# Kernel tuning notes

Hardware: AMD Instinct MI355X
Metric: run time of the kernel (lower is better)

Reference implementation:

```python
import jax, jax.numpy as jnp
import numpy as np

B, N, D = 16, 512, 256
PH, UH, UPH = 8, 4, 4          # P_GAT heads, U_GAT heads, UP_GAT heads
P_LAYERS, U_LAYERS = 2, 1
FH, NC = 128, 2                # final hidden, num classes
N_TRAIT = 4


def setup_inputs() -> dict:
    key = jax.random.key(0)
    keys = iter(jax.random.split(key, 64))

    def rn(shape, s=0.05):
        return jax.random.normal(next(keys), shape, dtype=jnp.float32) * s

    inp = {
        "p_mask": jnp.ones((B, N), jnp.float32),
        "feature": rn((B, N, D), 1.0),
        "c_node": rn((B, 1, D), 1.0),
        "pgat_W": rn((D, D)),
        "pgat_attn": rn((PH, 2 * (D // PH))),
    }
    for i in range(1, 5):
        inp[f"up{i}_qw"] = rn((D, D))
        inp[f"up{i}_qb"] = rn((D,))
        inp[f"up{i}_kw"] = rn((D, D))
        inp[f"up{i}_kb"] = rn((D,))
        inp[f"up{i}_ow"] = rn((D, D * UPH))
        inp[f"up{i}_ob"] = rn((D,))
    inp["ugat_W"] = rn((D, D))
    inp["ugat_attn"] = rn((UH, 2 * (D // UH)))
    inp["mlp_w1"] = rn((FH, D))
    inp["mlp_b1"] = rn((FH,))
    inp["mlp_w2"] = rn((FH, FH))
    inp["mlp_b2"] = rn((FH,))
    for i in range(1, 5):
        inp[f"fcf{i}_w"] = rn((NC, FH))
        inp[f"fcf{i}_b"] = rn((NC,))
    return inp


def _mh_gat(feature, W, attn_w, n_head, num_layers, adj=None):
    """Shared math of P_GAT / U_GAT.
    attn(cat([q_i, k_j]))[..., h, h] decomposes into q_i.wq_h + k_j.wk_h,
    identical math to the broadcast-concat-linear-diagonal in the source."""
    Bx, Nx, d = feature.shape
    dh = d // n_head
    wq, wk = attn_w[:, :dh], attn_w[:, dh:]           # [h, dh] each
    for _ in range(num_layers):
        qk = (feature @ W.T).reshape(Bx, Nx, n_head, dh)
        sq = jnp.einsum('bqhd,hd->bqh', qk, wq)
        sk = jnp.einsum('bkhd,hd->bkh', qk, wk)
        scores = jnp.tanh(sq[:, :, None, :] + sk[:, None, :, :])  # [B,q,k,h]
        if adj is not None:
            scores = jnp.where(adj[:, :, :, None] == 0, jnp.float32(-1e-8), scores)
        att = jax.nn.softmax(scores, axis=-2)          # softmax over k
        hid = jnp.tanh(jnp.einsum('bqkh,bkhd->bqhd', att, qk))
        feature = feature + hid.reshape(Bx, Nx, d)
    return feature


def _up_gat(p_mask, p_feat, u_feat, qw, qb, kw, kb, ow, ob):
    """UP_GAT: all heads/layers share params & inputs -> identical heads."""
    d = p_feat.shape[-1]
    q = u_feat @ qw.T + qb                             # [B,1,D]
    k = p_feat @ kw.T + kb                             # [B,Np,D]
    sim = jnp.einsum('bqd,bkd->bqk', q, k) / jnp.sqrt(jnp.float32(d))
    sim = jnp.where(p_mask[:, None, :] == 0, jnp.float32(1e-8), sim)
    att = jax.nn.softmax(sim, axis=2)
    head = att @ p_feat                                # [B,1,D]
    mh = jnp.concatenate([head] * UPH, axis=-1)        # concat of identical heads
    return (mh @ ow.T + ob)[:, 0, :]                   # squeeze(1)


def reference(p_mask, feature, c_node, pgat_W, pgat_attn,
              up1_qw, up1_qb, up1_kw, up1_kb, up1_ow, up1_ob,
              up2_qw, up2_qb, up2_kw, up2_kb, up2_ow, up2_ob,
              up3_qw, up3_qb, up3_kw, up3_kb, up3_ow, up3_ob,
              up4_qw, up4_qb, up4_kw, up4_kb, up4_ow, up4_ob,
              ugat_W, ugat_attn, mlp_w1, mlp_b1, mlp_w2, mlp_b2,
              fcf1_w, fcf1_b, fcf2_w, fcf2_b, fcf3_w, fcf3_b, fcf4_w, fcf4_b):
    Bx = p_mask.shape[0]
    adj = p_mask[:, :, None] * p_mask[:, None, :]      # [B,N,N]
    new_p = _mh_gat(feature, pgat_W, pgat_attn, PH, P_LAYERS, adj=adj)
    new_mask = jnp.concatenate([p_mask, jnp.ones((Bx, 1), p_mask.dtype)], axis=1)
    comb = jnp.concatenate([new_p, c_node], axis=1)    # [B,N+1,D]

    u1 = _up_gat(new_mask, comb, c_node, up1_qw, up1_qb, up1_kw, up1_kb, up1_ow, up1_ob)
    u2 = _up_gat(new_mask, comb, c_node, up2_qw, up2_qb, up2_kw, up2_kb, up2_ow, up2_ob)
    u3 = _up_gat(new_mask, comb, c_node, up3_qw, up3_qb, up3_kw, up3_kb, up3_ow, up3_ob)
    u4 = _up_gat(new_mask, comb, c_node, up4_qw, up4_qb, up4_kw, up4_kb, up4_ow, up4_ob)

    u = jnp.stack([u1, u2, u3, u4], axis=1)            # [B,4,D]
    u = _mh_gat(u, ugat_W, ugat_attn, UH, U_LAYERS, adj=None)

    def mlp(x):  # fcs1..4 share modules in the torch source
        h = jax.nn.relu(x @ mlp_w1.T + mlp_b1)
        return jax.nn.relu(h @ mlp_w2.T + mlp_b2)

    heads = [(fcf1_w, fcf1_b), (fcf2_w, fcf2_b), (fcf3_w, fcf3_b), (fcf4_w, fcf4_b)]
    logits = [mlp(u[:, i]) @ w.T + b for i, (w, b) in enumerate(heads)]
    return jnp.stack(logits, axis=0)                   # [4,B,NC]
```

## Files before the change

### kernel.cpp

```cpp
#include <hip/hip_runtime.h>

constexpr int CB   = 16;
constexpr int CN   = 512;
constexpr int CD   = 256;
constexpr int CPH  = 8;
constexpr int CDH  = 32;
constexpr int CNP1 = 513;
constexpr int CFH  = 128;
constexpr int CNC  = 2;

typedef __bf16 bf16x8 __attribute__((ext_vector_type(8)));
typedef __bf16 bf16x4 __attribute__((ext_vector_type(4)));
typedef float  f32x4  __attribute__((ext_vector_type(4)));

__device__ __forceinline__ float tanh_fast(float x) {
  x = fminf(fmaxf(x, -15.f), 15.f);
  float e = __expf(2.f * x);
  return (e - 1.f) / (e + 1.f);
}

__device__ __forceinline__ float exp2x_clamped(float x) {
  x = fminf(fmaxf(x, -18.f), 18.f);
  return __expf(2.f * x);
}

__global__ __launch_bounds__(256) void prep_wsplit(
    const float* __restrict__ W, bf16x8* __restrict__ wfH, bf16x8* __restrict__ wfL)
{
  const int id = blockIdx.x * 256 + threadIdx.x;
  const int row = id >> 5;
  const int c   = id & 31;
  const float* src = W + (size_t)row * CD + c * 8;
  float4 a0 = *(const float4*)src, a1 = *(const float4*)(src + 4);
  float v[8] = {a0.x, a0.y, a0.z, a0.w, a1.x, a1.y, a1.z, a1.w};
  bf16x8 hi, lo;
#pragma unroll
  for (int j = 0; j < 8; j++) {
    hi[j] = (__bf16)v[j];
    lo[j] = (__bf16)(v[j] - (float)hi[j]);
  }
  const int x = row >> 6, jj = (row >> 4) & 3, lc = row & 15;
  const int s = c >> 2, q = c & 3;
  const int idx = (((x * 8 + s) * 4 + jj) * 4 + q) * 16 + lc;
  wfH[idx] = hi;
  wfL[idx] = lo;
}

__global__ __launch_bounds__(256) void gemm_fused(
    const float* __restrict__ A,
    const bf16x8* __restrict__ wfH, const bf16x8* __restrict__ wfL,
    const float* __restrict__ attnw, __bf16* __restrict__ C,
    float* __restrict__ sqT, float* __restrict__ skT,
    const float* __restrict__ cnode,
    const float* __restrict__ qw0, const float* __restrict__ qb0,
    const float* __restrict__ kw0, const float* __restrict__ kb0,
    const float* __restrict__ ow0,
    const float* __restrict__ qw1, const float* __restrict__ qb1,
    const float* __restrict__ kw1, const float* __restrict__ kb1,
    const float* __restrict__ ow1,
    const float* __restrict__ qw2, const float* __restrict__ qb2,
    const float* __restrict__ kw2, const float* __restrict__ kb2,
    const float* __restrict__ ow2,
    const float* __restrict__ qw3, const float* __restrict__ qb3,
    const float* __restrict__ kw3, const float* __restrict__ kb3,
    const float* __restrict__ ow3,
    float* __restrict__ qt_, float* __restrict__ qkb,
    float* __restrict__ comb, float* __restrict__ head, float* __restrict__ den,
    float* __restrict__ weff)
{
  const int t  = threadIdx.x;

  __shared__ float s_cl[CD];
  __shared__ float s_ql[CD];
  __shared__ float s_red[256];

  if (blockIdx.y >= 128) {
    const int up = blockIdx.x, b = blockIdx.y - 128;
    const float* qw = (up == 0) ? qw0 : (up == 1) ? qw1 : (up == 2) ? qw2 : qw3;
    const float* qb = (up == 0) ? qb0 : (up == 1) ? qb1 : (up == 2) ? qb2 : qb3;
    const float* kw = (up == 0) ? kw0 : (up == 1) ? kw1 : (up == 2) ? kw2 : kw3;
    const float* kb = (up == 0) ? kb0 : (up == 1) ? kb1 : (up == 2) ? kb2 : kb3;
    const float* ow = (up == 0) ? ow0 : (up == 1) ? ow1 : (up == 2) ? ow2 : ow3;
    s_cl[t] = cnode[b * CD + t];
    head[((size_t)b * 4 + up) * CD + t] = 0.f;
    if (t == 0) den[b * 4 + up] = 0.f;
    {
#pragma unroll
      for (int i = 0; i < 4; i++) {
        int idx = t + 256 * i;
        int n = b * 16 + (idx >> 6), e4 = (idx & 63) * 4;
        const float* base = ow + (size_t)n * (4 * CD) + e4;
        float4 w0 = *(const float4*)(base);
        float4 w1 = *(const float4*)(base + CD);
        float4 w2 = *(const float4*)(base + 2 * CD);
        float4 w3 = *(const float4*)(base + 3 * CD);
        float4 o;
        o.x = w0.x + w1.x + w2.x + w3.x;
        o.y = w0.y + w1.y + w2.y + w3.y;
        o.z = w0.z + w1.z + w2.z + w3.z;
        o.w = w0.w + w1.w + w2.w + w3.w;
        *(float4*)(weff + (size_t)up * CD * CD + (size_t)n * CD + e4) = o;
      }
    }
    __syncthreads();
    if (up == 0) comb[((size_t)b * CNP1 + CN) * CD + t] = s_cl[t];
    {
      const float* wr = qw + (size_t)t * CD;
      float a = qb[t];
#pragma unroll 4
      for (int k = 0; k < CD; k += 4) {
        float4 w4 = *(const float4*)(wr + k);
        a += s_cl[k] * w4.x + s_cl[k + 1] * w4.y + s_cl[k + 2] * w4.z + s_cl[k + 3] * w4.w;
      }
      s_ql[t] = a;
    }
    __syncthreads();
    {
      float a0 = 0.f, a1 = 0.f, a2 = 0.f, a3 = 0.f;
#pragma unroll 4
      for (int d = 0; d < CD; d += 4) {
        a0 += s_ql[d]     * kw[(d)     * CD + t];
        a1 += s_ql[d + 1] * kw[(d + 1) * CD + t];
        a2 += s_ql[d + 2] * kw[(d + 2) * CD + t];
        a3 += s_ql[d + 3] * kw[(d + 3) * CD + t];
      }
      qt_[((size_t)up * CB + b) * CD + t] = (a0 + a1) + (a2 + a3);
    }
    s_red[t] = s_ql[t] * kb[t];
    __syncthreads();
    for (int s = 128; s > 0; s >>= 1) { if (t < s) s_red[t] += s_red[t + s]; __syncthreads(); }
    if (t == 0) qkb[up * CB + b] = s_red[0];
    return;
  }

  const int x  = blockIdx.x;
  const int nt = x * 64;
  const int mt = blockIdx.y * 64;
  const int wv = t >> 6, ln = t & 63;
  const int quad = ln >> 4, lc = ln & 15;

  f32x4 acc[4];
#pragma unroll
  for (int j = 0; j < 4; j++)
#pragma unroll
    for (int r = 0; r < 4; r++) acc[j][r] = 0.f;

  const float* ap = A + (size_t)(mt + wv * 16 + lc) * CD + quad * 8;

#pragma unroll 2
  for (int s = 0; s < 8; s++) {
    float4 a0 = *(const float4*)(ap + s * 32);
    float4 a1 = *(const float4*)(ap + s * 32 + 4);
    float av[8] = {a0.x, a0.y, a0.z, a0.w, a1.x, a1.y, a1.z, a1.w};
    bf16x8 ah, al;
#pragma unroll
    for (int j = 0; j < 8; j++) {
      ah[j] = (__bf16)av[j];
      al[j] = (__bf16)(av[j] - (float)ah[j]);
    }
    const int base = ((x * 8 + s) * 16 + quad) * 16 + lc;
#pragma unroll
    for (int j = 0; j < 4; j++) {
      bf16x8 bh = wfH[base + j * 64];
      bf16x8 bl = wfL[base + j * 64];
      acc[j] = __builtin_amdgcn_mfma_f32_16x16x32_bf16(ah, bh, acc[j], 0, 0, 0);
      acc[j] = __builtin_amdgcn_mfma_f32_16x16x32_bf16(ah, bl, acc[j], 0, 0, 0);
      acc[j] = __builtin_amdgcn_mfma_f32_16x16x32_bf16(al, bh, acc[j], 0, 0, 0);
    }
  }
#pragma unroll
  for (int j = 0; j < 4; j++)
#pragma unroll
    for (int r = 0; r < 4; r++)
      C[(size_t)(mt + wv * 16 + quad * 4 + r) * 256 + nt + j * 16 + lc] =
          (__bf16)acc[j][r];

  const int hA = blockIdx.x * 2, hB = hA + 1;
  const float wqa0 = attnw[hA * 64 + lc],      wqa1 = attnw[hA * 64 + 16 + lc];
  const float wka0 = attnw[hA * 64 + 32 + lc], wka1 = attnw[hA * 64 + 48 + lc];
  const float wqb0 = attnw[hB * 64 + lc],      wqb1 = attnw[hB * 64 + 16 + lc];
  const float wkb0 = attnw[hB * 64 + 32 + lc], wkb1 = attnw[hB * 64 + 48 + lc];
  float sqa[4], ska[4], sqb[4], skb[4];
#pragma unroll
  for (int r = 0; r < 4; r++) {
    sqa[r] = acc[0][r] * wqa0 + acc[1][r] * wqa1;
    ska[r] = acc[0][r] * wka0 + acc[1][r] * wka1;
    sqb[r] = acc[2][r] * wqb0 + acc[3][r] * wqb1;
    skb[r] = acc[2][r] * wkb0 + acc[3][r] * wkb1;
  }
#pragma unroll
  for (int m = 1; m <= 8; m <<= 1) {
#pragma unroll
    for (int r = 0; r < 4; r++) {
      sqa[r] += __shfl_xor(sqa[r], m);
      ska[r] += __shfl_xor(ska[r], m);
      sqb[r] += __shfl_xor(sqb[r], m);
      skb[r] += __shfl_xor(skb[r], m);
    }
  }
  if (lc == 0) {
#pragma unroll
    for (int r = 0; r < 4; r++) {
      int gm = mt + wv * 16 + quad * 4 + r;
      int bb = gm >> 9, nn = gm & 511;
      sqT[((size_t)bb * CPH + hA) * CN + nn] = sqa[r];
      skT[((size_t)bb * CPH + hA) * CN + nn] = ska[r];
      sqT[((size_t)bb * CPH + hB) * CN + nn] = sqb[r];
      skT[((size_t)bb * CPH + hB) * CN + nn] = skb[r];
    }
  }
}

__global__ __launch_bounds__(256) void pgat_attn3(
    const __bf16* __restrict__ qk, const float* __restrict__ sqT,
    const float* __restrict__ skT, const float* __restrict__ pmask,
    const float* __restrict__ fin, float* __restrict__ fout, int outStride)
{
  const int qt = blockIdx.x;
  const int h  = blockIdx.y;
  const int b  = blockIdx.z;
  const int t  = threadIdx.x;
  const int wv = t >> 6, ln = t & 63;
  const int quad = ln >> 4, lc = ln & 15;

  __shared__ __align__(16) __bf16 vslice[32][520];
  __shared__ float skl[CN];
  __shared__ float ckm[CN];
  __shared__ float sql64[64];

  for (int i = t; i < CN; i += 256) {
    skl[i] = exp2x_clamped(skT[((size_t)b * CPH + h) * CN + i]);
    ckm[i] = (pmask[b * CN + i] == 0.f) ? 0.f : 1.f;
  }
  if (t < 64) sql64[t] = exp2x_clamped(sqT[((size_t)b * CPH + h) * CN + qt * 64 + t]);
  for (int i = t; i < CN * 4; i += 256) {
    const int k = i >> 2, dq = (i & 3) * 8;
    bf16x8 v = *(const bf16x8*)(qk + ((size_t)(b * CN + k)) * CD + h * CDH + dq);
#pragma unroll
    for (int j = 0; j < 8; j++) vslice[dq + j][k] = v[j];
  }
  __syncthreads();

  const int q0 = qt * 64 + wv * 16;
  const float tq = sql64[wv * 16 + lc];
  const float qf = ckm[q0 + lc];

  f32x4 V0 = {0.f,0.f,0.f,0.f}, V1 = {0.f,0.f,0.f,0.f}, Dn = {0.f,0.f,0.f,0.f};
  bf16x8 ones;
#pragma unroll
  for (int j = 0; j < 8; j++) ones[j] = (__bf16)1.0f;

#pragma unroll 2
  for (int k0 = 0; k0 < CN; k0 += 32) {
    bf16x8 fa;
#pragma unroll
    for (int j = 0; j < 8; j++) {
      const int kk = k0 + quad * 8 + j;
      float u  = tq * skl[kk];
      float th = (u - 1.f) * __builtin_amdgcn_rcpf(u + 1.f);
      th *= qf * ckm[kk];
      fa[j] = (__bf16)__expf(th);
    }
    bf16x8 b0 = *(const bf16x8*)&vslice[lc][k0 + quad * 8];
    bf16x8 b1 = *(const bf16x8*)&vslice[16 + lc][k0 + quad * 8];
    V0 = __builtin_amdgcn_mfma_f32_16x16x32_bf16(fa, b0, V0, 0, 0, 0);
    V1 = __builtin_amdgcn_mfma_f32_16x16x32_bf16(fa, b1, V1, 0, 0, 0);
    Dn = __builtin_amdgcn_mfma_f32_16x16x32_bf16(fa, ones, Dn, 0, 0, 0);
  }

  const int d0 = h * CDH + lc;
#pragma unroll
  for (int r = 0; r < 4; r++) {
    const int q = q0 + quad * 4 + r;
    float inv = 1.f / Dn[r];
    const float* ip = fin + ((size_t)b * CN + q) * CD;
    float*       op = fout + ((size_t)b * outStride + q) * CD;
    op[d0]      = ip[d0]      + tanh_fast(V0[r] * inv);
    op[d0 + 16] = ip[d0 + 16] + tanh_fast(V1[r] * inv);
  }
}


__global__ __launch_bounds__(256) void up_headsim(
    const float* __restrict__ comb, const float* __restrict__ qt,
    const float* __restrict__ qkb, const float* __restrict__ pmask,
    float* __restrict__ head, float* __restrict__ den)
{
  const int b = blockIdx.x, n0 = blockIdx.y * 64, t = threadIdx.x;
  const int up = t >> 6, j = t & 63;
  __shared__ float qtl[4][CD];
  __shared__ float qkbl[4];
  __shared__ float attl[4][64];
  for (int i = t; i < 4 * CD; i += 256)
    qtl[i >> 8][i & 255] = qt[((size_t)(i >> 8) * CB + b) * CD + (i & 255)];
  if (t < 4) qkbl[t] = qkb[t * CB + b];
  __syncthreads();
  {
    const int n = n0 + j;
    float e = 0.f;
    if (n < CNP1) {
      const float* cr = comb + ((size_t)b * CNP1 + n) * CD;
      float p = 0.f;
#pragma unroll 4
      for (int d = 0; d < CD; d += 4) {
        float4 c4 = *(const float4*)(cr + d);
        p += qtl[up][d] * c4.x + qtl[up][d + 1] * c4.y
           + qtl[up][d + 2] * c4.z + qtl[up][d + 3] * c4.w;
      }
      float s = (p + qkbl[up]) * 0.0625f;
      float m = (n < CN) ? pmask[b * CN + n] : 1.f;
      if (m == 0.f) s = 1e-8f;
      e = __expf(s);
    }
    attl[up][j] = e;
  }
  __syncthreads();
  float4 acc = make_float4(0.f, 0.f, 0.f, 0.f);
  const int nmax = min(64, CNP1 - n0);
  for (int jj = 0; jj < nmax; jj++) {
    float a = attl[up][jj];
    float4 c4 = *(const float4*)(comb + ((size_t)b * CNP1 + n0 + jj) * CD + j * 4);
    acc.x += a * c4.x; acc.y += a * c4.y; acc.z += a * c4.z; acc.w += a * c4.w;
  }
  float* hp = head + ((size_t)b * 4 + up) * CD + j * 4;
  atomicAdd(hp + 0, acc.x); atomicAdd(hp + 1, acc.y);
  atomicAdd(hp + 2, acc.z); atomicAdd(hp + 3, acc.w);
  if (j == 0) {
    float s = 0.f;
    for (int jj = 0; jj < 64; jj++) s += attl[up][jj];
    atomicAdd(den + b * 4 + up, s);
  }
}

__global__ __launch_bounds__(256) void up_out_ugat(
    const float* __restrict__ head, const float* __restrict__ den,
    const float* __restrict__ weff,
    const float* __restrict__ ob0, const float* __restrict__ ob1,
    const float* __restrict__ ob2, const float* __restrict__ ob3,
    const float* __restrict__ ugat_W, const float* __restrict__ attnw,
    float* __restrict__ uout, float* __restrict__ uqk, float* __restrict__ sqk)
{
  const int b = blockIdx.x, up = blockIdx.y, t = threadIdx.x;
  const float* ob = (up == 0) ? ob0 : (up == 1) ? ob1 : (up == 2) ? ob2 : ob3;
  __shared__ float hl[CD];
  __shared__ float xl[CD];
  __shared__ float qkl[CD];
  hl[t] = head[((size_t)b * 4 + up) * CD + t] * (1.f / den[b * 4 + up]);
  __syncthreads();
  {
    const float* r0 = weff + (size_t)up * CD * CD + (size_t)t * CD;
    float p0 = 0.f, p1 = 0.f, p2 = 0.f, p3 = 0.f;
#pragma unroll 4
    for (int d = 0; d < CD; d += 16) {
      float4 w0 = *(const float4*)(r0 + d);
      float4 w1 = *(const float4*)(r0 + d + 4);
      float4 w2 = *(const float4*)(r0 + d + 8);
      float4 w3 = *(const float4*)(r0 + d + 12);
      p0 += hl[d +  0] * w0.x + hl[d +  1] * w0.y + hl[d +  2] * w0.z + hl[d +  3] * w0.w;
      p1 += hl[d +  4] * w1.x + hl[d +  5] * w1.y + hl[d +  6] * w1.z + hl[d +  7] * w1.w;
      p2 += hl[d +  8] * w2.x + hl[d +  9] * w2.y + hl[d + 10] * w2.z + hl[d + 11] * w2.w;
      p3 += hl[d + 12] * w3.x + hl[d + 13] * w3.y + hl[d + 14] * w3.z + hl[d + 15] * w3.w;
    }
    float a = ob[t] + ((p0 + p1) + (p2 + p3));
    xl[t] = a;
    uout[((size_t)b * 4 + up) * CD + t] = a;
  }
  __syncthreads();
  {
    const float* wr = ugat_W + (size_t)t * CD;
    float p0 = 0.f, p1 = 0.f, p2 = 0.f, p3 = 0.f;
#pragma unroll 4
    for (int d = 0; d < CD; d += 16) {
      float4 w0 = *(const float4*)(wr + d);
      float4 w1 = *(const float4*)(wr + d + 4);
      float4 w2 = *(const float4*)(wr + d + 8);
      float4 w3 = *(const float4*)(wr + d + 12);
      p0 += xl[d +  0] * w0.x + xl[d +  1] * w0.y + xl[d +  2] * w0.z + xl[d +  3] * w0.w;
      p1 += xl[d +  4] * w1.x + xl[d +  5] * w1.y + xl[d +  6] * w1.z + xl[d +  7] * w1.w;
      p2 += xl[d +  8] * w2.x + xl[d +  9] * w2.y + xl[d + 10] * w2.z + xl[d + 11] * w2.w;
      p3 += xl[d + 12] * w3.x + xl[d + 13] * w3.y + xl[d + 14] * w3.z + xl[d + 15] * w3.w;
    }
    float a = (p0 + p1) + (p2 + p3);
    qkl[t] = a;
    uqk[((size_t)b * 4 + up) * CD + t] = a;
  }
  __syncthreads();
  if (t < 8) {
    const int h = t >> 1, which = t & 1;
    const float* w = attnw + h * 128 + which * 64;
    float s = 0.f;
    for (int j = 0; j < 64; j++) s += qkl[h * 64 + j] * w[j];
    sqk[(((size_t)b * 4 + up) * 4 + h) * 2 + which] = s;
  }
}

__global__ __launch_bounds__(256) void ugat_mlp2(
    const float* __restrict__ u, const float* __restrict__ uqk,
    const float* __restrict__ sqk,
    const float* __restrict__ w1, const float* __restrict__ b1,
    const float* __restrict__ w2, const float* __restrict__ b2,
    const float* __restrict__ f1w, const float* __restrict__ f1b,
    const float* __restrict__ f2w, const float* __restrict__ f2b,
    const float* __restrict__ f3w, const float* __restrict__ f3b,
    const float* __restrict__ f4w, const float* __restrict__ f4b,
    float* __restrict__ out)
{
  const int b = blockIdx.x, trait = blockIdx.y, t = threadIdx.x;
  __shared__ float uq[4][CD];
  __shared__ float sl[4][4], kl[4][4];
  __shared__ float xl[CD];
  __shared__ float h1[CFH];
  __shared__ float h2[CFH];
  for (int i = t; i < 4 * CD; i += 256) uq[i >> 8][i & 255] = uqk[(size_t)b * 4 * CD + i];
  if (t < 16) {
    int node = t >> 2, h = t & 3;
    sl[node][h] = sqk[(((size_t)b * 4 + node) * 4 + h) * 2 + 0];
    kl[node][h] = sqk[(((size_t)b * 4 + node) * 4 + h) * 2 + 1];
  }
  float ur = u[((size_t)b * 4 + trait) * CD + t];
  __syncthreads();
  {
    const int h = t >> 6;
    float e[4]; float ssum = 0.f;
#pragma unroll
    for (int k = 0; k < 4; k++) { e[k] = __expf(tanh_fast(sl[trait][h] + kl[k][h])); ssum += e[k]; }
    float hid = 0.f;
#pragma unroll
    for (int k = 0; k < 4; k++) hid += e[k] * uq[k][t];
    xl[t] = ur + tanh_fast(hid / ssum);
  }
  __syncthreads();
  if (t < CFH) {
    const float* r = w1 + (size_t)t * CD;
    float a = b1[t];
#pragma unroll 4
    for (int k = 0; k < CD; k += 4) {
      float4 v = *(const float4*)(r + k);
      a += xl[k] * v.x + xl[k + 1] * v.y + xl[k + 2] * v.z + xl[k + 3] * v.w;
    }
    h1[t] = fmaxf(a, 0.f);
  }
  __syncthreads();
  if (t < CFH) {
    const float* r = w2 + (size_t)t * CFH;
    float a = b2[t];
#pragma unroll 4
    for (int k = 0; k < CFH; k += 4) {
      float4 v = *(const float4*)(r + k);
      a += h1[k] * v.x + h1[k + 1] * v.y + h1[k + 2] * v.z + h1[k + 3] * v.w;
    }
    h2[t] = fmaxf(a, 0.f);
  }
  __syncthreads();
  if (t < CNC) {
    const float* fw; const float* fb;
    switch (trait) {
      case 0:  fw = f1w; fb = f1b; break;
      case 1:  fw = f2w; fb = f2b; break;
      case 2:  fw = f3w; fb = f3b; break;
      default: fw = f4w; fb = f4b; break;
    }
    const float* r = fw + (size_t)t * CFH;
    float a = fb[t];
    for (int k = 0; k < CFH; k++) a += h2[k] * r[k];
    out[(size_t)trait * (CB * CNC) + b * CNC + t] = a;
  }
}

extern "C" void kernel_launch(void* const* d_in, const int* in_sizes, int n_in,
                              void* d_out, int out_size, void* d_ws, size_t ws_size,
                              hipStream_t stream) {
  (void)in_sizes; (void)n_in; (void)out_size; (void)ws_size;
  const float* pmask    = (const float*)d_in[0];
  const float* feature  = (const float*)d_in[1];
  const float* cnode    = (const float*)d_in[2];
  const float* pgat_W   = (const float*)d_in[3];
  const float* pgat_att = (const float*)d_in[4];
  const float* upw[4][6];
  for (int i = 0; i < 4; i++)
    for (int j = 0; j < 6; j++) upw[i][j] = (const float*)d_in[5 + i * 6 + j];
  const float* ugat_W   = (const float*)d_in[29];
  const float* ugat_att = (const float*)d_in[30];
  const float* mlp_w1 = (const float*)d_in[31];
  const float* mlp_b1 = (const float*)d_in[32];
  const float* mlp_w2 = (const float*)d_in[33];
  const float* mlp_b2 = (const float*)d_in[34];
  const float* fcf[8];
  for (int j = 0; j < 8; j++) fcf[j] = (const float*)d_in[35 + j];

  float* ws = (float*)d_ws;
  size_t o = 0;
  float* ws_qk   = ws + o; o += (size_t)CB * CN * CD;
  float* ws_feat = ws + o; o += (size_t)CB * CN * CD;
  float* ws_comb = ws + o; o += (size_t)CB * CNP1 * CD;
  float* ws_sq   = ws + o; o += (size_t)CB * CPH * CN;
  float* ws_sk   = ws + o; o += (size_t)CB * CPH * CN;
  float* ws_qt   = ws + o; o += (size_t)4 * CB * CD;
  float* ws_qkb  = ws + o; o += 4 * CB;
  float* ws_den  = ws + o; o += CB * 4;
  float* ws_head = ws + o; o += (size_t)CB * 4 * CD;
  float* ws_u    = ws + o; o += (size_t)CB * 4 * CD;
  float* ws_uqk  = ws + o; o += (size_t)CB * 4 * CD;
  float* ws_sqk  = ws + o; o += (size_t)CB * 4 * 4 * 2;
  float* ws_weff = ws + o; o += (size_t)4 * CD * CD;
  float* ws_wfh  = ws + o; o += (size_t)CD * CD / 2;
  float* ws_wfl  = ws + o; o += (size_t)CD * CD / 2;
  __bf16* qk16 = (__bf16*)ws_qk;
  bf16x8* wfH = (bf16x8*)ws_wfh;
  bf16x8* wfL = (bf16x8*)ws_wfl;

  const dim3 gemmGrid1(CD / 64, (CB * CN) / 64 + 16);
  const dim3 gemmGrid2(CD / 64, (CB * CN) / 64);
  const dim3 attnGrid(CN / 64, CPH, CB);

  prep_wsplit<<<dim3(32), 256, 0, stream>>>(pgat_W, wfH, wfL);

  gemm_fused<<<gemmGrid1, 256, 0, stream>>>(feature, wfH, wfL, pgat_att, qk16, ws_sq, ws_sk,
      cnode,
      upw[0][0], upw[0][1], upw[0][2], upw[0][3], upw[0][4],
      upw[1][0], upw[1][1], upw[1][2], upw[1][3], upw[1][4],
      upw[2][0], upw[2][1], upw[2][2], upw[2][3], upw[2][4],
      upw[3][0], upw[3][1], upw[3][2], upw[3][3], upw[3][4],
      ws_qt, ws_qkb, ws_comb, ws_head, ws_den, ws_weff);
  pgat_attn3<<<attnGrid, 256, 0, stream>>>(qk16, ws_sq, ws_sk, pmask, feature, ws_feat, CN);
  gemm_fused<<<gemmGrid2, 256, 0, stream>>>(ws_feat, wfH, wfL, pgat_att, qk16, ws_sq, ws_sk,
      cnode,
      upw[0][0], upw[0][1], upw[0][2], upw[0][3], upw[0][4],
      upw[1][0], upw[1][1], upw[1][2], upw[1][3], upw[1][4],
      upw[2][0], upw[2][1], upw[2][2], upw[2][3], upw[2][4],
      upw[3][0], upw[3][1], upw[3][2], upw[3][3], upw[3][4],
      ws_qt, ws_qkb, ws_comb, ws_head, ws_den, ws_weff);
  pgat_attn3<<<attnGrid, 256, 0, stream>>>(qk16, ws_sq, ws_sk, pmask, ws_feat, ws_comb, CNP1);

  up_headsim<<<dim3(CB, (CNP1 + 63) / 64), 256, 0, stream>>>(ws_comb, ws_qt, ws_qkb, pmask,
                                                             ws_head, ws_den);
  up_out_ugat<<<dim3(CB, 4), 256, 0, stream>>>(ws_head, ws_den, ws_weff,
      upw[0][5], upw[1][5], upw[2][5], upw[3][5],
      ugat_W, ugat_att, ws_u, ws_uqk, ws_sqk);

  ugat_mlp2<<<dim3(CB, 4), 256, 0, stream>>>(ws_u, ws_uqk, ws_sqk,
                                             mlp_w1, mlp_b1, mlp_w2, mlp_b2,
                                             fcf[0], fcf[1], fcf[2], fcf[3],
                                             fcf[4], fcf[5], fcf[6], fcf[7],
                                             (float*)d_out);
}
```

Baseline: 268.1 us.

## Split weights inside GEMM via LDS tiles and fuse UP-out with U_GAT tail

Removes the separate weight-split prep kernel. The GEMM now loads A and W tiles per K-step, converts them to bf16 hi/lo pairs, stages them in shared memory and reads MFMA fragments from there. It also merges the UP output projection and the U_GAT/MLP head into one kernel, so each block recomputes all four u vectors instead of passing them through workspace buffers. This saves two launches at the cost of redundant tail work per trait block and extra syncs and LDS traffic in the GEMM.

```diff
diff --git a/kernel.cpp b/kernel.cpp
--- a/kernel.cpp
+++ b/kernel.cpp
@@ -24,31 +24,8 @@
   return __expf(2.f * x);
 }
 
-__global__ __launch_bounds__(256) void prep_wsplit(
-    const float* __restrict__ W, bf16x8* __restrict__ wfH, bf16x8* __restrict__ wfL)
-{
-  const int id = blockIdx.x * 256 + threadIdx.x;
-  const int row = id >> 5;
-  const int c   = id & 31;
-  const float* src = W + (size_t)row * CD + c * 8;
-  float4 a0 = *(const float4*)src, a1 = *(const float4*)(src + 4);
-  float v[8] = {a0.x, a0.y, a0.z, a0.w, a1.x, a1.y, a1.z, a1.w};
-  bf16x8 hi, lo;
-#pragma unroll
-  for (int j = 0; j < 8; j++) {
-    hi[j] = (__bf16)v[j];
-    lo[j] = (__bf16)(v[j] - (float)hi[j]);
-  }
-  const int x = row >> 6, jj = (row >> 4) & 3, lc = row & 15;
-  const int s = c >> 2, q = c & 3;
-  const int idx = (((x * 8 + s) * 4 + jj) * 4 + q) * 16 + lc;
-  wfH[idx] = hi;
-  wfL[idx] = lo;
-}
-
 __global__ __launch_bounds__(256) void gemm_fused(
-    const float* __restrict__ A,
-    const bf16x8* __restrict__ wfH, const bf16x8* __restrict__ wfL,
+    const float* __restrict__ A, const float* __restrict__ W,
     const float* __restrict__ attnw, __bf16* __restrict__ C,
     float* __restrict__ sqT, float* __restrict__ skT,
     const float* __restrict__ cnode,
@@ -70,6 +47,10 @@
 {
   const int t  = threadIdx.x;
 
+  __shared__ __align__(16) __bf16 aHi[64][56];
+  __shared__ __align__(16) __bf16 aLo[64][56];
+  __shared__ __align__(16) __bf16 bHi[64][56];
+  __shared__ __align__(16) __bf16 bLo[64][56];
   __shared__ float s_cl[CD];
   __shared__ float s_ql[CD];
   __shared__ float s_red[256];
@@ -133,8 +114,7 @@
     return;
   }
 
-  const int x  = blockIdx.x;
-  const int nt = x * 64;
+  const int nt = blockIdx.x * 64;
   const int mt = blockIdx.y * 64;
   const int wv = t >> 6, ln = t & 63;
   const int quad = ln >> 4, lc = ln & 15;
@@ -145,27 +125,41 @@
 #pragma unroll
     for (int r = 0; r < 4; r++) acc[j][r] = 0.f;
 
-  const float* ap = A + (size_t)(mt + wv * 16 + lc) * CD + quad * 8;
-
-#pragma unroll 2
-  for (int s = 0; s < 8; s++) {
-    float4 a0 = *(const float4*)(ap + s * 32);
-    float4 a1 = *(const float4*)(ap + s * 32 + 4);
-    float av[8] = {a0.x, a0.y, a0.z, a0.w, a1.x, a1.y, a1.z, a1.w};
-    bf16x8 ah, al;
-#pragma unroll
-    for (int j = 0; j < 8; j++) {
-      ah[j] = (__bf16)av[j];
-      al[j] = (__bf16)(av[j] - (float)ah[j]);
-    }
-    const int base = ((x * 8 + s) * 16 + quad) * 16 + lc;
+  const int sr  = t >> 2;
+  const int skq = (t & 3) * 8;
+
+  for (int k0 = 0; k0 < 256; k0 += 32) {
+    __syncthreads();
+    {
+      const float* ap = A + (size_t)(mt + sr) * 256 + k0 + skq;
+      const float* wp = W + (size_t)(nt + sr) * 256 + k0 + skq;
+      float4 a0 = *(const float4*)ap, a1 = *(const float4*)(ap + 4);
+      float4 w0 = *(const float4*)wp, w1 = *(const float4*)(wp + 4);
+      float av[8] = {a0.x, a0.y, a0.z, a0.w, a1.x, a1.y, a1.z, a1.w};
+      float wvv[8] = {w0.x, w0.y, w0.z, w0.w, w1.x, w1.y, w1.z, w1.w};
+      bf16x8 ah, al, bh, bl;
+#pragma unroll
+      for (int j = 0; j < 8; j++) {
+        ah[j] = (__bf16)av[j];
+        al[j] = (__bf16)(av[j] - (float)ah[j]);
+        bh[j] = (__bf16)wvv[j];
+        bl[j] = (__bf16)(wvv[j] - (float)bh[j]);
+      }
+      *(bf16x8*)&aHi[sr][skq] = ah;
+      *(bf16x8*)&aLo[sr][skq] = al;
+      *(bf16x8*)&bHi[sr][skq] = bh;
+      *(bf16x8*)&bLo[sr][skq] = bl;
+    }
+    __syncthreads();
+    bf16x8 fah = *(const bf16x8*)&aHi[wv * 16 + lc][quad * 8];
+    bf16x8 fal = *(const bf16x8*)&aLo[wv * 16 + lc][quad * 8];
 #pragma unroll
     for (int j = 0; j < 4; j++) {
-      bf16x8 bh = wfH[base + j * 64];
-      bf16x8 bl = wfL[base + j * 64];
-      acc[j] = __builtin_amdgcn_mfma_f32_16x16x32_bf16(ah, bh, acc[j], 0, 0, 0);
-      acc[j] = __builtin_amdgcn_mfma_f32_16x16x32_bf16(ah, bl, acc[j], 0, 0, 0);
-      acc[j] = __builtin_amdgcn_mfma_f32_16x16x32_bf16(al, bh, acc[j], 0, 0, 0);
+      bf16x8 fbh = *(const bf16x8*)&bHi[j * 16 + lc][quad * 8];
+      bf16x8 fbl = *(const bf16x8*)&bLo[j * 16 + lc][quad * 8];
+      acc[j] = __builtin_amdgcn_mfma_f32_16x16x32_bf16(fah, fbh, acc[j], 0, 0, 0);
+      acc[j] = __builtin_amdgcn_mfma_f32_16x16x32_bf16(fah, fbl, acc[j], 0, 0, 0);
+      acc[j] = __builtin_amdgcn_mfma_f32_16x16x32_bf16(fal, fbh, acc[j], 0, 0, 0);
     }
   }
 #pragma unroll
@@ -332,71 +326,12 @@
   }
 }
 
-__global__ __launch_bounds__(256) void up_out_ugat(
+__global__ __launch_bounds__(256) void ugat_tail(
     const float* __restrict__ head, const float* __restrict__ den,
     const float* __restrict__ weff,
     const float* __restrict__ ob0, const float* __restrict__ ob1,
     const float* __restrict__ ob2, const float* __restrict__ ob3,
     const float* __restrict__ ugat_W, const float* __restrict__ attnw,
-    float* __restrict__ uout, float* __restrict__ uqk, float* __restrict__ sqk)
-{
-  const int b = blockIdx.x, up = blockIdx.y, t = threadIdx.x;
-  const float* ob = (up == 0) ? ob0 : (up == 1) ? ob1 : (up == 2) ? ob2 : ob3;
-  __shared__ float hl[CD];
-  __shared__ float xl[CD];
-  __shared__ float qkl[CD];
-  hl[t] = head[((size_t)b * 4 + up) * CD + t] * (1.f / den[b * 4 + up]);
-  __syncthreads();
-  {
-    const float* r0 = weff + (size_t)up * CD * CD + (size_t)t * CD;
-    float p0 = 0.f, p1 = 0.f, p2 = 0.f, p3 = 0.f;
-#pragma unroll 4
-    for (int d = 0; d < CD; d += 16) {
-      float4 w0 = *(const float4*)(r0 + d);
-      float4 w1 = *(const float4*)(r0 + d + 4);
-      float4 w2 = *(const float4*)(r0 + d + 8);
-      float4 w3 = *(const float4*)(r0 + d + 12);
-      p0 += hl[d +  0] * w0.x + hl[d +  1] * w0.y + hl[d +  2] * w0.z + hl[d +  3] * w0.w;
-      p1 += hl[d +  4] * w1.x + hl[d +  5] * w1.y + hl[d +  6] * w1.z + hl[d +  7] * w1.w;
-      p2 += hl[d +  8] * w2.x + hl[d +  9] * w2.y + hl[d + 10] * w2.z + hl[d + 11] * w2.w;
-      p3 += hl[d + 12] * w3.x + hl[d + 13] * w3.y + hl[d + 14] * w3.z + hl[d + 15] * w3.w;
-    }
-    float a = ob[t] + ((p0 + p1) + (p2 + p3));
-    xl[t] = a;
-    uout[((size_t)b * 4 + up) * CD + t] = a;
-  }
-  __syncthreads();
-  {
-    const float* wr = ugat_W + (size_t)t * CD;
-    float p0 = 0.f, p1 = 0.f, p2 = 0.f, p3 = 0.f;
-#pragma unroll 4
-    for (int d = 0; d < CD; d += 16) {
-      float4 w0 = *(const float4*)(wr + d);
-      float4 w1 = *(const float4*)(wr + d + 4);
-      float4 w2 = *(const float4*)(wr + d + 8);
-      float4 w3 = *(const float4*)(wr + d + 12);
-      p0 += xl[d +  0] * w0.x + xl[d +  1] * w0.y + xl[d +  2] * w0.z + xl[d +  3] * w0.w;
-      p1 += xl[d +  4] * w1.x + xl[d +  5] * w1.y + xl[d +  6] * w1.z + xl[d +  7] * w1.w;
-      p2 += xl[d +  8] * w2.x + xl[d +  9] * w2.y + xl[d + 10] * w2.z + xl[d + 11] * w2.w;
-      p3 += xl[d + 12] * w3.x + xl[d + 13] * w3.y + xl[d + 14] * w3.z + xl[d + 15] * w3.w;
-    }
-    float a = (p0 + p1) + (p2 + p3);
-    qkl[t] = a;
-    uqk[((size_t)b * 4 + up) * CD + t] = a;
-  }
-  __syncthreads();
-  if (t < 8) {
-    const int h = t >> 1, which = t & 1;
-    const float* w = attnw + h * 128 + which * 64;
-    float s = 0.f;
-    for (int j = 0; j < 64; j++) s += qkl[h * 64 + j] * w[j];
-    sqk[(((size_t)b * 4 + up) * 4 + h) * 2 + which] = s;
-  }
-}
-
-__global__ __launch_bounds__(256) void ugat_mlp2(
-    const float* __restrict__ u, const float* __restrict__ uqk,
-    const float* __restrict__ sqk,
     const float* __restrict__ w1, const float* __restrict__ b1,
     const float* __restrict__ w2, const float* __restrict__ b2,
     const float* __restrict__ f1w, const float* __restrict__ f1b,
@@ -406,18 +341,62 @@
     float* __restrict__ out)
 {
   const int b = blockIdx.x, trait = blockIdx.y, t = threadIdx.x;
+  __shared__ float hl[4][CD];
+  __shared__ float xs[4][CD];
   __shared__ float uq[4][CD];
   __shared__ float sl[4][4], kl[4][4];
   __shared__ float xl[CD];
   __shared__ float h1[CFH];
   __shared__ float h2[CFH];
-  for (int i = t; i < 4 * CD; i += 256) uq[i >> 8][i & 255] = uqk[(size_t)b * 4 * CD + i];
-  if (t < 16) {
-    int node = t >> 2, h = t & 3;
-    sl[node][h] = sqk[(((size_t)b * 4 + node) * 4 + h) * 2 + 0];
-    kl[node][h] = sqk[(((size_t)b * 4 + node) * 4 + h) * 2 + 1];
-  }
-  float ur = u[((size_t)b * 4 + trait) * CD + t];
+
+#pragma unroll
+  for (int u = 0; u < 4; u++)
+    hl[u][t] = head[((size_t)b * 4 + u) * CD + t] * (1.f / den[b * 4 + u]);
+  __syncthreads();
+#pragma unroll 1
+  for (int u = 0; u < 4; u++) {
+    const float* ob = (u == 0) ? ob0 : (u == 1) ? ob1 : (u == 2) ? ob2 : ob3;
+    const float* r0 = weff + (size_t)u * CD * CD + (size_t)t * CD;
+    float p0 = 0.f, p1 = 0.f, p2 = 0.f, p3 = 0.f;
+#pragma unroll 4
+    for (int d = 0; d < CD; d += 16) {
+      float4 w0 = *(const float4*)(r0 + d);
+      float4 w1v = *(const float4*)(r0 + d + 4);
+      float4 w2v = *(const float4*)(r0 + d + 8);
+      float4 w3 = *(const float4*)(r0 + d + 12);
+      p0 += hl[u][d +  0] * w0.x + hl[u][d +  1] * w0.y + hl[u][d +  2] * w0.z + hl[u][d +  3] * w0.w;
+      p1 += hl[u][d +  4] * w1v.x + hl[u][d +  5] * w1v.y + hl[u][d +  6] * w1v.z + hl[u][d +  7] * w1v.w;
+      p2 += hl[u][d +  8] * w2v.x + hl[u][d +  9] * w2v.y + hl[u][d + 10] * w2v.z + hl[u][d + 11] * w2v.w;
+      p3 += hl[u][d + 12] * w3.x + hl[u][d + 13] * w3.y + hl[u][d + 14] * w3.z + hl[u][d + 15] * w3.w;
+    }
+    xs[u][t] = ob[t] + ((p0 + p1) + (p2 + p3));
+  }
+  __syncthreads();
+#pragma unroll 1
+  for (int u = 0; u < 4; u++) {
+    const float* wr = ugat_W + (size_t)t * CD;
+    float p0 = 0.f, p1 = 0.f, p2 = 0.f, p3 = 0.f;
+#pragma unroll 4
+    for (int d = 0; d < CD; d += 16) {
+      float4 w0 = *(const float4*)(wr + d);
+      float4 w1v = *(const float4*)(wr + d + 4);
+      float4 w2v = *(const float4*)(wr + d + 8);
+      float4 w3 = *(const float4*)(wr + d + 12);
+      p0 += xs[u][d +  0] * w0.x + xs[u][d +  1] * w0.y + xs[u][d +  2] * w0.z + xs[u][d +  3] * w0.w;
+      p1 += xs[u][d +  4] * w1v.x + xs[u][d +  5] * w1v.y + xs[u][d +  6] * w1v.z + xs[u][d +  7] * w1v.w;
+      p2 += xs[u][d +  8] * w2v.x + xs[u][d +  9] * w2v.y + xs[u][d + 10] * w2v.z + xs[u][d + 11] * w2v.w;
+      p3 += xs[u][d + 12] * w3.x + xs[u][d + 13] * w3.y + xs[u][d + 14] * w3.z + xs[u][d + 15] * w3.w;
+    }
+    uq[u][t] = (p0 + p1) + (p2 + p3);
+  }
+  __syncthreads();
+  if (t < 32) {
+    const int node = t >> 3, h = (t >> 1) & 3, which = t & 1;
+    const float* w = attnw + h * 128 + which * 64;
+    float s = 0.f;
+    for (int j = 0; j < 64; j++) s += uq[node][h * 64 + j] * w[j];
+    if (which == 0) sl[node][h] = s; else kl[node][h] = s;
+  }
   __syncthreads();
   {
     const int h = t >> 6;
@@ -427,7 +406,7 @@
     float hid = 0.f;
 #pragma unroll
     for (int k = 0; k < 4; k++) hid += e[k] * uq[k][t];
-    xl[t] = ur + tanh_fast(hid / ssum);
+    xl[t] = xs[trait][t] + tanh_fast(hid / ssum);
   }
   __syncthreads();
   if (t < CFH) {
@@ -499,23 +478,14 @@
   float* ws_qkb  = ws + o; o += 4 * CB;
   float* ws_den  = ws + o; o += CB * 4;
   float* ws_head = ws + o; o += (size_t)CB * 4 * CD;
-  float* ws_u    = ws + o; o += (size_t)CB * 4 * CD;
-  float* ws_uqk  = ws + o; o += (size_t)CB * 4 * CD;
-  float* ws_sqk  = ws + o; o += (size_t)CB * 4 * 4 * 2;
   float* ws_weff = ws + o; o += (size_t)4 * CD * CD;
-  float* ws_wfh  = ws + o; o += (size_t)CD * CD / 2;
-  float* ws_wfl  = ws + o; o += (size_t)CD * CD / 2;
   __bf16* qk16 = (__bf16*)ws_qk;
-  bf16x8* wfH = (bf16x8*)ws_wfh;
-  bf16x8* wfL = (bf16x8*)ws_wfl;
 
   const dim3 gemmGrid1(CD / 64, (CB * CN) / 64 + 16);
   const dim3 gemmGrid2(CD / 64, (CB * CN) / 64);
   const dim3 attnGrid(CN / 64, CPH, CB);
 
-  prep_wsplit<<<dim3(32), 256, 0, stream>>>(pgat_W, wfH, wfL);
-
-  gemm_fused<<<gemmGrid1, 256, 0, stream>>>(feature, wfH, wfL, pgat_att, qk16, ws_sq, ws_sk,
+  gemm_fused<<<gemmGrid1, 256, 0, stream>>>(feature, pgat_W, pgat_att, qk16, ws_sq, ws_sk,
       cnode,
       upw[0][0], upw[0][1], upw[0][2], upw[0][3], upw[0][4],
       upw[1][0], upw[1][1], upw[1][2], upw[1][3], upw[1][4],
@@ -523,7 +493,7 @@
       upw[3][0], upw[3][1], upw[3][2], upw[3][3], upw[3][4],
       ws_qt, ws_qkb, ws_comb, ws_head, ws_den, ws_weff);
   pgat_attn3<<<attnGrid, 256, 0, stream>>>(qk16, ws_sq, ws_sk, pmask, feature, ws_feat, CN);
-  gemm_fused<<<gemmGrid2, 256, 0, stream>>>(ws_feat, wfH, wfL, pgat_att, qk16, ws_sq, ws_sk,
+  gemm_fused<<<gemmGrid2, 256, 0, stream>>>(ws_feat, pgat_W, pgat_att, qk16, ws_sq, ws_sk,
       cnode,
       upw[0][0], upw[0][1], upw[0][2], upw[0][3], upw[0][4],
       upw[1][0], upw[1][1], upw[1][2], upw[1][3], upw[1][4],
@@ -534,13 +504,11 @@
 
   up_headsim<<<dim3(CB, (CNP1 + 63) / 64), 256, 0, stream>>>(ws_comb, ws_qt, ws_qkb, pmask,
                                                              ws_head, ws_den);
-  up_out_ugat<<<dim3(CB, 4), 256, 0, stream>>>(ws_head, ws_den, ws_weff,
+  ugat_tail<<<dim3(CB, 4), 256, 0, stream>>>(ws_head, ws_den, ws_weff,
       upw[0][5], upw[1][5], upw[2][5], upw[3][5],
-      ugat_W, ugat_att, ws_u, ws_uqk, ws_sqk);
-
-  ugat_mlp2<<<dim3(CB, 4), 256, 0, stream>>>(ws_u, ws_uqk, ws_sqk,
-                                             mlp_w1, mlp_b1, mlp_w2, mlp_b2,
-                                             fcf[0], fcf[1], fcf[2], fcf[3],
-                                             fcf[4], fcf[5], fcf[6], fcf[7],
-                                             (float*)d_out);
-}
+      ugat_W, ugat_att,
+      mlp_w1, mlp_b1, mlp_w2, mlp_b2,
+      fcf[0], fcf[1], fcf[2], fcf[3],
+      fcf[4], fcf[5], fcf[6], fcf[7],
+      (float*)d_out);
+}
```

Result: slower. 297.7 us (+11.0%).
